# Optimization experiments

Measured on AMD Instinct MI355X. Metric: run time of the kernel, lower is better.

Reference implementation:

```python
import jax, jax.numpy as jnp
import numpy as np

BN_EPS = 1e-5

def conv3d(x, w, b):
    # standard 3D conv, stride 1, pad 1, NCDHW
    out = jax.lax.conv_general_dilated(x, w, (1, 1, 1), ((1, 1), (1, 1), (1, 1)),
                                       dimension_numbers=('NCDHW', 'OIDHW', 'NCDHW'))
    return out + b[None, :, None, None, None]

def batchnorm(x, gamma, beta):
    # training-mode BN over (B, D, H, W) per channel
    mu = x.mean(axis=(0, 2, 3, 4), keepdims=True)
    var = x.var(axis=(0, 2, 3, 4), keepdims=True)
    g = gamma[None, :, None, None, None]
    b = beta[None, :, None, None, None]
    return g * (x - mu) * jax.lax.rsqrt(var + BN_EPS) + b

def deform_conv3d(x, offset, weight, cpg):
    # x: [B,C,D,H,W]; offset: [B, G*27*3, D,H,W] with layout [B,G,27,(d,h,w),D,H,W]
    # weight: [C_out, C_in, 3,3,3]; kernel 3, stride 1, pad 1 -> same spatial size
    B, C, D, H, W = x.shape
    G = C // cpg
    off = offset.reshape(B, G, 27, 3, D, H, W)
    k = jnp.arange(27)
    kd = (k // 9 - 1).astype(x.dtype).reshape(1, 1, 27, 1, 1, 1)
    kh = ((k // 3) % 3 - 1).astype(x.dtype).reshape(1, 1, 27, 1, 1, 1)
    kw = (k % 3 - 1).astype(x.dtype).reshape(1, 1, 27, 1, 1, 1)
    gd = jnp.arange(D, dtype=x.dtype).reshape(1, 1, 1, D, 1, 1)
    gh = jnp.arange(H, dtype=x.dtype).reshape(1, 1, 1, 1, H, 1)
    gw = jnp.arange(W, dtype=x.dtype).reshape(1, 1, 1, 1, 1, W)
    # fractional sampling positions per (batch, group, tap, voxel): [B,G,27,D,H,W]
    pd = gd + kd + off[:, :, :, 0]
    ph = gh + kh + off[:, :, :, 1]
    pw = gw + kw + off[:, :, :, 2]
    d0 = jnp.floor(pd); h0 = jnp.floor(ph); w0 = jnp.floor(pw)
    fd = pd - d0; fh = ph - h0; fw = pw - w0
    d0i = d0.astype(jnp.int32); h0i = h0.astype(jnp.int32); w0i = w0.astype(jnp.int32)
    xg = x.reshape(B, G, cpg, D * H * W)
    N = 27 * D * H * W
    acc = jnp.zeros((B, G, cpg, 27, D, H, W), x.dtype)
    for dd in (0, 1):
        for hh in (0, 1):
            for ww in (0, 1):
                di = d0i + dd; hi = h0i + hh; wi = w0i + ww
                wgt = ((fd if dd else 1.0 - fd) * (fh if hh else 1.0 - fh)
                       * (fw if ww else 1.0 - fw))
                valid = ((di >= 0) & (di < D) & (hi >= 0) & (hi < H)
                         & (wi >= 0) & (wi < W))  # zero padding outside
                dic = jnp.clip(di, 0, D - 1)
                hic = jnp.clip(hi, 0, H - 1)
                wic = jnp.clip(wi, 0, W - 1)
                idx = ((dic * H + hic) * W + wic).reshape(B, G, 1, N)
                vals = jnp.take_along_axis(xg, jnp.broadcast_to(idx, (B, G, cpg, N)), axis=3)
                vals = vals.reshape(B, G, cpg, 27, D, H, W)
                acc = acc + (wgt * valid)[:, :, None] * vals
    wr = weight.reshape(weight.shape[0], G, cpg, 27)
    return jnp.einsum('bgckdhw,ogck->bodhw', acc, wr)

def setup_inputs() -> dict:
    key = jax.random.key(0)
    ks = jax.random.split(key, 8)
    B, C, D, H, W = 2, 64, 8, 32, 32
    cpg = 8
    Coff = (C // cpg) * 3 * 27  # 648
    fan = 1.0 / np.sqrt(C * 27)
    x = jax.random.normal(ks[0], (B, C, D, H, W), jnp.float32)
    w_off1 = jax.random.normal(ks[1], (Coff, C, 3, 3, 3), jnp.float32) * 0.01
    b_off1 = jnp.zeros((Coff,), jnp.float32)
    w1 = jax.random.normal(ks[2], (C, C, 3, 3, 3), jnp.float32) * fan
    g1 = jnp.ones((C,), jnp.float32)
    be1 = jnp.zeros((C,), jnp.float32)
    w_off2 = jax.random.normal(ks[3], (Coff, C, 3, 3, 3), jnp.float32) * 0.01
    b_off2 = jnp.zeros((Coff,), jnp.float32)
    w2 = jax.random.normal(ks[4], (C, C, 3, 3, 3), jnp.float32) * fan
    g2 = jnp.ones((C,), jnp.float32)
    be2 = jnp.zeros((C,), jnp.float32)
    return {'x': x, 'w_off1': w_off1, 'b_off1': b_off1, 'w1': w1, 'g1': g1,
            'be1': be1, 'w_off2': w_off2, 'b_off2': b_off2, 'w2': w2,
            'g2': g2, 'be2': be2, 'cpg': cpg}

def reference(x, w_off1, b_off1, w1, g1, be1, w_off2, b_off2, w2, g2, be2, cpg):
    off1 = conv3d(x, w_off1, b_off1)
    out = deform_conv3d(x, off1, w1, cpg)
    out = jax.nn.relu(batchnorm(out, g1, be1))
    off2 = conv3d(x, w_off2, b_off2)  # note: offsets computed from x, as in source
    out = deform_conv3d(out, off2, w2, cpg)
    out = batchnorm(out, g2, be2) + x
    out = jax.nn.relu(out)
    return (out, off1, off2)
```

## Files before the change

### kernel.cpp

```cpp
#include <hip/hip_runtime.h>
#include <stdint.h>

typedef unsigned short u16;
typedef __attribute__((ext_vector_type(8))) short bf16x8;
typedef __attribute__((ext_vector_type(4))) float f32x4;

#define DEV static __device__ __forceinline__

#define BB    2
#define CC    64
#define DDD   8
#define HHH   32
#define WWW   32
#define DHW   8192
#define MTOT  16384
#define GG    8
#define KTOT  1728
#define NOFF  1296
#define NOFFP 1408
#define COFF  648

#define OFF1_ELEM (BB*CC*DHW)
#define OFF2_ELEM (OFF1_ELEM + BB*COFF*DHW)

#define XCL_OFF   0ull
#define YCL_OFF   2097152ull
#define WOFF_OFF  4194304ull
#define W1_OFF    9060352ull
#define W2_OFF    9281536ull
#define C1_OFF    9502720ull
#define C2_OFF    13697024ull
#define ST1_OFF   17891328ull
#define ST2_OFF   17891840ull
#define ZPG_OFF   17892352ull
#define PART_OFF  17892608ull

DEV float bf2f(u16 u){ union { uint32_t i; float f; } v; v.i = ((uint32_t)u) << 16; return v.f; }
DEV u16 f2bf(float f){ union { float f; uint32_t i; } v; v.f = f;
  uint32_t r = v.i + 0x7fffu + ((v.i >> 16) & 1u); return (u16)(r >> 16); }

DEV void gld16(const void* g, void* l){
  __builtin_amdgcn_global_load_lds((const __attribute__((address_space(1))) void*)g,
                                   (__attribute__((address_space(3))) void*)l, 16, 0, 0);
}

#define PRE0 (BB*CC*DHW)
#define PRE1 (PRE0 + NOFFP*KTOT)
#define PRE2 (PRE1 + CC*KTOT)
#define PRE3 (PRE2 + CC*KTOT)
#define PRETOT (PRE3 + 128)

__global__ void k_prep(const float* __restrict__ x,
                       const float* __restrict__ wo1, const float* __restrict__ wo2,
                       const float* __restrict__ w1, const float* __restrict__ w2,
                       u16* __restrict__ xcl, u16* __restrict__ woff,
                       u16* __restrict__ w1b, u16* __restrict__ w2b,
                       u16* __restrict__ zpg)
{
  int idx = blockIdx.x * 256 + threadIdx.x;
  if (idx < PRE0) {
    int p = idx & (DHW - 1);
    int c = (idx >> 13) & 63;
    int b = idx >> 19;
    xcl[(size_t)(b * DHW + p) * CC + c] = f2bf(x[idx]);
  } else if (idx < PRE1) {
    int j = idx - PRE0;
    int k = j % KTOT, n = j / KTOT;
    int tap = k >> 6, cin = k & 63;
    float v = 0.f;
    if (n < NOFF) {
      const float* w = (n < COFF) ? wo1 : wo2;
      int nn = (n < COFF) ? n : n - COFF;
      v = w[(size_t)nn * KTOT + cin * 27 + tap];
    }
    woff[j] = f2bf(v);
  } else if (idx < PRE2) {
    int j = idx - PRE1;
    int k = j % KTOT, n = j / KTOT;
    int tap = k >> 6, cin = k & 63;
    w1b[j] = f2bf(w1[(size_t)n * KTOT + cin * 27 + tap]);
  } else if (idx < PRE3) {
    int j = idx - PRE2;
    int k = j % KTOT, n = j / KTOT;
    int tap = k >> 6, cin = k & 63;
    w2b[j] = f2bf(w2[(size_t)n * KTOT + cin * 27 + tap]);
  } else if (idx < PRETOT) {
    zpg[idx - PRE3] = 0;
  }
}

__global__ __launch_bounds__(256) void k_gemm_off(
    const u16* __restrict__ xcl, const u16* __restrict__ woff,
    const float* __restrict__ boff1, const float* __restrict__ boff2,
    float* __restrict__ dout, const u16* __restrict__ zpg)
{
  __shared__ u16 Al[128 * 64];
  __shared__ u16 Bl[128 * 64];
  const int tid = threadIdx.x;
  const int wv = tid >> 6, lane = tid & 63;
  const int m0 = blockIdx.x * 128;
  const int n0 = blockIdx.y * 128;
  const int lr = lane >> 3, lc = lane & 7;
  const int lcs = (lc ^ lr) << 3;
  const int b  = m0 >> 13;
  const int p0 = m0 & (DHW - 1);
  int ad[4], ah[4], aw[4];
  #pragma unroll
  for (int i = 0; i < 4; ++i) {
    int p = p0 + wv * 32 + i * 8 + lr;
    ad[i] = p >> 10; ah[i] = (p >> 5) & 31; aw[i] = p & 31;
  }
  const size_t xb = (size_t)b * DHW * CC;

  f32x4 acc[4][4] = {};
  const int wm = wv >> 1, wn = wv & 1;
  const int r16 = lane & 15, q = lane >> 4;
  const int rs = r16 & 7;
  const int nbase = n0 + wn * 64;
  const int jlim = (nbase >= NOFF) ? 0 : ((NOFF - nbase >= 64) ? 4 : ((NOFF - nbase + 15) >> 4));

  for (int t = 0; t < 27; ++t) {
    int kd = t / 9 - 1, kh = (t / 3) % 3 - 1, kw = t % 3 - 1;
    #pragma unroll
    for (int i = 0; i < 4; ++i) {
      int d2 = ad[i] + kd, h2 = ah[i] + kh, w2 = aw[i] + kw;
      bool ok = ((unsigned)d2 < DDD) & ((unsigned)h2 < HHH) & ((unsigned)w2 < WWW);
      const u16* src = ok ? (xcl + xb + (size_t)((d2 << 10) + (h2 << 5) + w2) * CC + lcs)
                          : zpg;
      gld16(src, &Al[(wv * 32 + i * 8) * 64]);
    }
    #pragma unroll
    for (int i = 0; i < 4; ++i) {
      int r = wv * 32 + i * 8 + lr;
      const u16* src = woff + (size_t)(n0 + r) * KTOT + t * 64 + lcs;
      gld16(src, &Bl[(wv * 32 + i * 8) * 64]);
    }
    __syncthreads();
    #pragma unroll
    for (int kk = 0; kk < 2; ++kk) {
      const int cs = ((kk * 4 + q) ^ rs) << 3;
      bf16x8 af[4];
      #pragma unroll
      for (int i = 0; i < 4; ++i)
        af[i] = *(const bf16x8*)&Al[(wm * 64 + i * 16 + r16) * 64 + cs];
      #pragma unroll
      for (int j = 0; j < 4; ++j) {
        if (j < jlim) {
          bf16x8 bfr = *(const bf16x8*)&Bl[(wn * 64 + j * 16 + r16) * 64 + cs];
          #pragma unroll
          for (int i = 0; i < 4; ++i)
            acc[i][j] = __builtin_amdgcn_mfma_f32_16x16x32_bf16(af[i], bfr, acc[i][j], 0, 0, 0);
        }
      }
    }
    __syncthreads();
  }

  float biasj[4]; int ncj[4];
  #pragma unroll
  for (int j = 0; j < 4; ++j) {
    int nc = n0 + wn * 64 + j * 16 + r16;
    ncj[j] = nc;
    biasj[j] = (nc < NOFF) ? ((nc < COFF) ? boff1[nc] : boff2[nc - COFF]) : 0.f;
  }
  #pragma unroll
  for (int i = 0; i < 4; ++i) {
    int mrow = m0 + wm * 64 + i * 16 + q * 4;
    int bb = mrow >> 13, p = mrow & (DHW - 1);
    #pragma unroll
    for (int j = 0; j < 4; ++j) {
      int nc = ncj[j];
      if (nc < NOFF) {
        int ch = (nc < COFF) ? nc : nc - COFF;
        size_t base = (nc < COFF) ? (size_t)OFF1_ELEM : (size_t)OFF2_ELEM;
        f32x4 v = acc[i][j] + biasj[j];
        *(f32x4*)(dout + base + ((size_t)(bb * COFF + ch)) * DHW + p) = v;
      }
    }
  }
}

__global__ __launch_bounds__(256) void k_deform(
    const u16* __restrict__ src, const float* __restrict__ offs,
    const u16* __restrict__ wB, float* __restrict__ cdst,
    const u16* __restrict__ zpg)
{
  __shared__ u16 Al[2 * 16 * 64];
  __shared__ u16 Bl[2 * 64 * 64];
  const int tid = threadIdx.x;
  const int wv = tid >> 6, lane = tid & 63;
  const int mrow0 = blockIdx.x * 16;
  const int b  = mrow0 >> 13;
  const int p0 = mrow0 & (DHW - 1);

  const int pl = tid & 15;
  const int g  = (tid >> 4) & 7;
  const int th = tid >> 7;
  const int p  = p0 + pl;
  const int d = p >> 10, h = (p >> 5) & 31, w = p & 31;
  const u16* sb = src + (size_t)b * DHW * CC + g * 8;
  const size_t obase = ((size_t)(b * COFF + g * 81)) * DHW + p;
  u16* awp = &Al[th * 1024 + pl * 64 + ((g ^ (pl & 7)) << 3)];

  const int lr = lane >> 3, lc = lane & 7;
  const int lcs = (lc ^ lr) << 3;

  f32x4 acc = {};
  const int r16 = lane & 15, q = lane >> 4;
  const int rs = r16 & 7;

  for (int ph = 0; ph < 14; ++ph) {
    #pragma unroll
    for (int i = 0; i < 4; ++i) {
      int tb = 2 * ph + (i >> 1);
      int row = (i & 1) * 32 + wv * 8 + lr;
      const u16* s = (tb < 27) ? (wB + (size_t)row * KTOT + tb * 64 + lcs) : zpg;
      gld16(s, &Bl[(i >> 1) * 4096 + (((i & 1) * 32 + wv * 8) * 64)]);
    }
    {
      int t = 2 * ph + th;
      float a8[8] = {0.f,0.f,0.f,0.f,0.f,0.f,0.f,0.f};
      if (t < 27) {
        int kd = t / 9 - 1, kh = (t / 3) % 3 - 1, kw = t % 3 - 1;
        size_t ob = obase + (size_t)(t * 3) * DHW;
        float pd = (float)(d + kd) + offs[ob];
        float phh = (float)(h + kh) + offs[ob + DHW];
        float pw = (float)(w + kw) + offs[ob + 2 * DHW];
        float fd0 = floorf(pd), fh0 = floorf(phh), fw0 = floorf(pw);
        float fd = pd - fd0, fh = phh - fh0, fw = pw - fw0;
        int d0 = (int)fd0, h0 = (int)fh0, w0 = (int)fw0;
        #pragma unroll
        for (int dd = 0; dd < 2; ++dd) {
          float wd = dd ? fd : 1.f - fd;
          int di = d0 + dd;
          #pragma unroll
          for (int hh = 0; hh < 2; ++hh) {
            float wh = hh ? fh : 1.f - fh;
            int hi = h0 + hh;
            #pragma unroll
            for (int ww = 0; ww < 2; ++ww) {
              int wi = w0 + ww;
              if (((unsigned)di < DDD) && ((unsigned)hi < HHH) && ((unsigned)wi < WWW)) {
                float wgt = wd * wh * (ww ? fw : 1.f - fw);
                bf16x8 v = *(const bf16x8*)(sb + (size_t)((di << 10) + (hi << 5) + wi) * CC);
                #pragma unroll
                for (int c = 0; c < 8; ++c) a8[c] += wgt * bf2f((u16)v[c]);
              }
            }
          }
        }
      }
      union { bf16x8 v; u16 u[8]; } o;
      #pragma unroll
      for (int c = 0; c < 8; ++c) o.u[c] = f2bf(a8[c]);
      *(bf16x8*)awp = o.v;
    }
    __syncthreads();
    #pragma unroll
    for (int tt = 0; tt < 2; ++tt) {
      #pragma unroll
      for (int kk = 0; kk < 2; ++kk) {
        const int cs = ((kk * 4 + q) ^ rs) << 3;
        bf16x8 af = *(const bf16x8*)&Al[tt * 1024 + r16 * 64 + cs];
        bf16x8 bf_ = *(const bf16x8*)&Bl[tt * 4096 + (wv * 16 + r16) * 64 + cs];
        acc = __builtin_amdgcn_mfma_f32_16x16x32_bf16(af, bf_, acc, 0, 0, 0);
      }
    }
    __syncthreads();
  }

  {
    int nc = wv * 16 + r16;
    int mr = mrow0 + q * 4;
    #pragma unroll
    for (int r = 0; r < 4; ++r)
      cdst[(size_t)(mr + r) * CC + nc] = acc[r];
  }
}

__global__ void k_bnpart(const float* __restrict__ c, float* __restrict__ part)
{
  int k = blockIdx.x, tid = threadIdx.x;
  int ch = tid & 63, sub = tid >> 6;
  float s = 0.f, s2 = 0.f;
  for (int mm = sub; mm < 64; mm += 4) {
    float v = c[(size_t)(k * 64 + mm) * CC + ch];
    s += v; s2 += v * v;
  }
  __shared__ float sh[4][128];
  sh[sub][ch] = s; sh[sub][64 + ch] = s2;
  __syncthreads();
  if (tid < 128)
    part[(size_t)k * 128 + tid] = sh[0][tid] + sh[1][tid] + sh[2][tid] + sh[3][tid];
}

__global__ void k_bnfin(const float* __restrict__ part, const float* __restrict__ gamma,
                        const float* __restrict__ beta, float* __restrict__ stats)
{
  int n = threadIdx.x;
  float S = 0.f, S2 = 0.f;
  for (int k = 0; k < 256; ++k) {
    S  += part[(size_t)k * 128 + n];
    S2 += part[(size_t)k * 128 + 64 + n];
  }
  float mu = S / (float)MTOT;
  float var = S2 / (float)MTOT - mu * mu;
  float sc = gamma[n] / sqrtf(var + 1e-5f);
  stats[n] = sc;
  stats[64 + n] = beta[n] - mu * sc;
}

__global__ void k_apply1(const float* __restrict__ c1, const float* __restrict__ st,
                         u16* __restrict__ ycl)
{
  int idx = blockIdx.x * 256 + threadIdx.x;
  if (idx >= MTOT * CC) return;
  int n = idx & 63;
  float v = st[n] * c1[idx] + st[64 + n];
  ycl[idx] = f2bf(fmaxf(v, 0.f));
}

__global__ void k_apply2(const float* __restrict__ c2, const float* __restrict__ st,
                         const float* __restrict__ x, float* __restrict__ out)
{
  int idx = blockIdx.x * 256 + threadIdx.x;
  if (idx >= BB * CC * DHW) return;
  int p = idx & (DHW - 1);
  int n = (idx >> 13) & 63;
  int b = idx >> 19;
  float v = st[n] * c2[(size_t)(b * DHW + p) * CC + n] + st[64 + n] + x[idx];
  out[idx] = fmaxf(v, 0.f);
}

extern "C" void kernel_launch(void* const* d_in, const int* in_sizes, int n_in,
                              void* d_out, int out_size, void* d_ws, size_t ws_size,
                              hipStream_t stream)
{
  (void)in_sizes; (void)n_in; (void)out_size; (void)ws_size;
  const float* x      = (const float*)d_in[0];
  const float* w_off1 = (const float*)d_in[1];
  const float* b_off1 = (const float*)d_in[2];
  const float* w1     = (const float*)d_in[3];
  const float* g1     = (const float*)d_in[4];
  const float* be1    = (const float*)d_in[5];
  const float* w_off2 = (const float*)d_in[6];
  const float* b_off2 = (const float*)d_in[7];
  const float* w2     = (const float*)d_in[8];
  const float* g2     = (const float*)d_in[9];
  const float* be2    = (const float*)d_in[10];

  char* ws = (char*)d_ws;
  u16*   xcl  = (u16*)(ws + XCL_OFF);
  u16*   ycl  = (u16*)(ws + YCL_OFF);
  u16*   woff = (u16*)(ws + WOFF_OFF);
  u16*   w1b  = (u16*)(ws + W1_OFF);
  u16*   w2b  = (u16*)(ws + W2_OFF);
  float* c1   = (float*)(ws + C1_OFF);
  float* c2   = (float*)(ws + C2_OFF);
  float* st1  = (float*)(ws + ST1_OFF);
  float* st2  = (float*)(ws + ST2_OFF);
  u16*   zpg  = (u16*)(ws + ZPG_OFF);
  float* part = (float*)(ws + PART_OFF);
  float* out  = (float*)d_out;

  k_prep<<<(PRETOT + 255) / 256, 256, 0, stream>>>(
      x, w_off1, w_off2, w1, w2, xcl, woff, w1b, w2b, zpg);

  k_gemm_off<<<dim3(MTOT / 128, NOFFP / 128), 256, 0, stream>>>(
      xcl, woff, b_off1, b_off2, out, zpg);

  k_deform<<<MTOT / 16, 256, 0, stream>>>(xcl, out + OFF1_ELEM, w1b, c1, zpg);
  k_bnpart<<<256, 256, 0, stream>>>(c1, part);
  k_bnfin<<<1, 64, 0, stream>>>(part, g1, be1, st1);
  k_apply1<<<(MTOT * CC) / 256, 256, 0, stream>>>(c1, st1, ycl);

  k_deform<<<MTOT / 16, 256, 0, stream>>>(ycl, out + OFF2_ELEM, w2b, c2, zpg);
  k_bnpart<<<256, 256, 0, stream>>>(c2, part);
  k_bnfin<<<1, 64, 0, stream>>>(part, g2, be2, st2);
  k_apply2<<<(BB*CC*DHW) / 256, 256, 0, stream>>>(c2, st2, x, out);
}
```

Before: 259.9 us.

## Unguard offset GEMM MFMA loop, remap deform thread lanes, widen BN finalize

The offset-conv GEMM drops its per-warp column-limit guard. It now loads all four B fragments up front and issues the full 4x4 MFMA grid unconditionally, which also does work on the padded columns beyond NOFF. The deformable kernel swaps the thread-to-(position, group) mapping so consecutive lanes cover different channel groups, aiming for better gather coalescing and a different LDS write pattern. The BN finalize kernel uses 128 threads, with sum and sum-of-squares reduced in parallel and combined through shared memory.

Result: faster. 250.6 us (-3.6%).

```diff
diff --git a/kernel.cpp b/kernel.cpp
--- a/kernel.cpp
+++ b/kernel.cpp
@@ -116,8 +116,6 @@
   const int wm = wv >> 1, wn = wv & 1;
   const int r16 = lane & 15, q = lane >> 4;
   const int rs = r16 & 7;
-  const int nbase = n0 + wn * 64;
-  const int jlim = (nbase >= NOFF) ? 0 : ((NOFF - nbase >= 64) ? 4 : ((NOFF - nbase + 15) >> 4));
 
   for (int t = 0; t < 27; ++t) {
     int kd = t / 9 - 1, kh = (t / 3) % 3 - 1, kw = t % 3 - 1;
@@ -139,19 +137,18 @@
     #pragma unroll
     for (int kk = 0; kk < 2; ++kk) {
       const int cs = ((kk * 4 + q) ^ rs) << 3;
-      bf16x8 af[4];
+      bf16x8 af[4], bfr[4];
       #pragma unroll
       for (int i = 0; i < 4; ++i)
         af[i] = *(const bf16x8*)&Al[(wm * 64 + i * 16 + r16) * 64 + cs];
       #pragma unroll
-      for (int j = 0; j < 4; ++j) {
-        if (j < jlim) {
-          bf16x8 bfr = *(const bf16x8*)&Bl[(wn * 64 + j * 16 + r16) * 64 + cs];
-          #pragma unroll
-          for (int i = 0; i < 4; ++i)
-            acc[i][j] = __builtin_amdgcn_mfma_f32_16x16x32_bf16(af[i], bfr, acc[i][j], 0, 0, 0);
-        }
-      }
+      for (int j = 0; j < 4; ++j)
+        bfr[j] = *(const bf16x8*)&Bl[(wn * 64 + j * 16 + r16) * 64 + cs];
+      #pragma unroll
+      for (int i = 0; i < 4; ++i)
+        #pragma unroll
+        for (int j = 0; j < 4; ++j)
+          acc[i][j] = __builtin_amdgcn_mfma_f32_16x16x32_bf16(af[i], bfr[j], acc[i][j], 0, 0, 0);
     }
     __syncthreads();
   }
@@ -193,9 +190,9 @@
   const int b  = mrow0 >> 13;
   const int p0 = mrow0 & (DHW - 1);
 
-  const int pl = tid & 15;
-  const int g  = (tid >> 4) & 7;
   const int th = tid >> 7;
+  const int pl = (tid >> 3) & 15;
+  const int g  = tid & 7;
   const int p  = p0 + pl;
   const int d = p >> 10, h = (p >> 5) & 31, w = p & 31;
   const u16* sb = src + (size_t)b * DHW * CC + g * 8;
@@ -297,17 +294,19 @@
 __global__ void k_bnfin(const float* __restrict__ part, const float* __restrict__ gamma,
                         const float* __restrict__ beta, float* __restrict__ stats)
 {
-  int n = threadIdx.x;
-  float S = 0.f, S2 = 0.f;
-  for (int k = 0; k < 256; ++k) {
-    S  += part[(size_t)k * 128 + n];
-    S2 += part[(size_t)k * 128 + 64 + n];
-  }
-  float mu = S / (float)MTOT;
-  float var = S2 / (float)MTOT - mu * mu;
-  float sc = gamma[n] / sqrtf(var + 1e-5f);
-  stats[n] = sc;
-  stats[64 + n] = beta[n] - mu * sc;
+  int tid = threadIdx.x;
+  float S = 0.f;
+  for (int k = 0; k < 256; ++k) S += part[(size_t)k * 128 + tid];
+  __shared__ float sh[128];
+  sh[tid] = S;
+  __syncthreads();
+  if (tid < 64) {
+    float mu = sh[tid] / (float)MTOT;
+    float var = sh[64 + tid] / (float)MTOT - mu * mu;
+    float sc = gamma[tid] / sqrtf(var + 1e-5f);
+    stats[tid] = sc;
+    stats[64 + tid] = beta[tid] - mu * sc;
+  }
 }
 
 __global__ void k_apply1(const float* __restrict__ c1, const float* __restrict__ st,
@@ -371,11 +370,11 @@
 
   k_deform<<<MTOT / 16, 256, 0, stream>>>(xcl, out + OFF1_ELEM, w1b, c1, zpg);
   k_bnpart<<<256, 256, 0, stream>>>(c1, part);
-  k_bnfin<<<1, 64, 0, stream>>>(part, g1, be1, st1);
+  k_bnfin<<<1, 128, 0, stream>>>(part, g1, be1, st1);
   k_apply1<<<(MTOT * CC) / 256, 256, 0, stream>>>(c1, st1, ycl);
 
   k_deform<<<MTOT / 16, 256, 0, stream>>>(ycl, out + OFF2_ELEM, w2b, c2, zpg);
   k_bnpart<<<256, 256, 0, stream>>>(c2, part);
-  k_bnfin<<<1, 64, 0, stream>>>(part, g2, be2, st2);
+  k_bnfin<<<1, 128, 0, stream>>>(part, g2, be2, st2);
   k_apply2<<<(BB*CC*DHW) / 256, 256, 0, stream>>>(c2, st2, x, out);
 }
```
